# Performance work log

Hardware: AMD Instinct MI355X
Metric: run time of the kernel (lower is better)

## Reference

```python
import jax, jax.numpy as jnp
import numpy as np

# Poincare ball hyperbolic multi-head attention (hypll-style HMultiheadAttention)
C = 1.0          # ball curvature
SQRT_C = 1.0
EPS = 1e-7
B, S, E, H = 4, 1024, 512, 8
HD = E // H      # head_dim = 64


def _project_to_ball(u, scale=0.5):
    n = jnp.linalg.norm(u, axis=-1, keepdims=True)
    return u * (scale / (1.0 + n))  # guarantees ||x|| < scale < 1/sqrt(C)


def h_linear(x, z, r):
    """Poincare fully-connected layer (Shimizu et al. HNN++), as in hypll HLinear.
    x: [..., n] points in the ball, z: [n, m] weight directions, r: [m] bias."""
    x2 = jnp.sum(x * x, -1, keepdims=True)
    lam = 2.0 / jnp.maximum(1.0 - C * x2, EPS)          # conformal factor lambda_x
    zn = jnp.maximum(jnp.linalg.norm(z, axis=0), EPS)    # [m]
    xz = x @ z                                           # [..., m]
    two_cr = 2.0 * SQRT_C * r
    v = (2.0 * zn / SQRT_C) * jnp.arcsinh(
        SQRT_C * lam * xz / zn * jnp.cosh(two_cr) - (lam - 1.0) * jnp.sinh(two_cr)
    )
    v2 = jnp.sum(v * v, -1, keepdims=True)
    return v / (1.0 + jnp.sqrt(1.0 + C * v2))            # map back into the ball


def _split_heads(x):
    b, s, e = x.shape
    return x.reshape(b, s, H, HD).transpose(0, 2, 1, 3)  # [B,H,S,hd]; matches split(dim=-1)


def _h_attention(q, k, v):
    # similarity = -poincare_dist(q, k), pairwise via the arccosh closed form
    # (avoids materializing a [B,H,Sq,Sk,hd] mobius_add tensor)
    q2 = jnp.sum(q * q, -1)[..., :, None]                # [B,H,Sq,1]
    k2 = jnp.sum(k * k, -1)[..., None, :]                # [B,H,1,Sk]
    qk = jnp.einsum('bhqd,bhkd->bhqk', q, k)
    diff2 = jnp.maximum(q2 + k2 - 2.0 * qk, 0.0)
    denom = jnp.maximum((1.0 - C * q2) * (1.0 - C * k2), EPS)
    arg = 1.0 + 2.0 * C * diff2 / denom
    dist = jnp.arccosh(jnp.maximum(arg, 1.0 + EPS)) / SQRT_C
    w = jax.nn.softmax(-dist, axis=-1)                   # attention_activation
    # attention_midpoint: weighted Mobius gyromidpoint then half scalar-mul
    v2 = jnp.sum(v * v, -1)                              # [B,H,Sk]
    lam = 2.0 / jnp.maximum(1.0 - C * v2, EPS)
    num = jnp.einsum('bhqk,bhkd->bhqd', w * lam[..., None, :], v)
    den = jnp.einsum('bhqk,bhk->bhq', w, lam - 1.0)[..., None]
    m_bar = num / jnp.where(jnp.abs(den) < EPS, EPS, den)
    mn = jnp.maximum(jnp.linalg.norm(m_bar, axis=-1, keepdims=True), EPS)
    t = jnp.minimum(SQRT_C * mn, 1.0 - 1e-6)
    return jnp.tanh(0.5 * jnp.arctanh(t)) * m_bar / (SQRT_C * mn)  # (1/2) mobius-scalar-mul


def setup_inputs() -> dict:
    key = jax.random.key(0)
    ks = jax.random.split(key, 9)
    query = _project_to_ball(jax.random.normal(ks[0], (B, S, E), jnp.float32))
    key_t = _project_to_ball(jax.random.normal(ks[1], (B, S, E), jnp.float32))
    value = _project_to_ball(jax.random.normal(ks[2], (B, S, E), jnp.float32))
    scale = E ** -0.5
    zq = jax.random.normal(ks[3], (E, E), jnp.float32) * scale
    zk = jax.random.normal(ks[4], (E, E), jnp.float32) * scale
    zv = jax.random.normal(ks[5], (E, E), jnp.float32) * scale
    rq = jax.random.normal(ks[6], (E,), jnp.float32) * 0.01
    rk = jax.random.normal(ks[7], (E,), jnp.float32) * 0.01
    rv = jax.random.normal(ks[8], (E,), jnp.float32) * 0.01
    return {"query": query, "key": key_t, "value": value,
            "zq": zq, "rq": rq, "zk": zk, "rk": rk, "zv": zv, "rv": rv}


def reference(query, key, value, zq, rq, zk, rk, zv, rv):
    pq = h_linear(query, zq, rq)
    pk = h_linear(key, zk, rk)
    pv = h_linear(value, zv, rv)
    q, k, v = _split_heads(pq), _split_heads(pk), _split_heads(pv)
    out = _h_attention(q, k, v)                          # [B,H,S,hd]
    return out.transpose(0, 2, 1, 3).reshape(B, S, E)    # manifold.cat over heads
```

## Files before the change

kernel.cpp:

```cpp
#include <hip/hip_runtime.h>
#include <hip/hip_bf16.h>
#include <math.h>

#define EPSf 1e-7f
typedef unsigned short u16;
typedef __attribute__((ext_vector_type(8))) short bf16x8;
typedef __attribute__((ext_vector_type(4))) float f32x4;

__device__ __forceinline__ float bf2f(u16 u) {
  union { unsigned int i; float f; } x; x.i = ((unsigned int)u) << 16; return x.f;
}
__device__ __forceinline__ u16 f2bf(float f) {
  union { float f; unsigned int i; } x; x.f = f;
  unsigned int r = x.i + 0x7fffu + ((x.i >> 16) & 1u);
  return (u16)(r >> 16);
}
__device__ __forceinline__ void gll16(const void* g, void* l) {
  __builtin_amdgcn_global_load_lds((__attribute__((address_space(1))) void*)(g),
                                   (__attribute__((address_space(3))) void*)(l),
                                   16, 0, 0);
}

__global__ __launch_bounds__(256) void prep(
    const float* __restrict__ xq, const float* __restrict__ xk, const float* __restrict__ xv,
    const float* __restrict__ zq, const float* __restrict__ zk, const float* __restrict__ zv,
    u16* __restrict__ Xh, u16* __restrict__ Xl,
    float* __restrict__ Xn, float* __restrict__ Vn,
    u16* __restrict__ ZhT, u16* __restrict__ ZlT, float* __restrict__ Zn) {
  __shared__ float tile[64][68];
  const int t = threadIdx.x;
  if (blockIdx.x < 6144) {
    const int gr = blockIdx.x * 2 + (t >> 7);
    const int mat = gr >> 12, row = gr & 4095;
    const float* X = (mat == 0) ? xq : (mat == 1) ? xk : xv;
    const int f4 = t & 127;
    float4 x = ((const float4*)(X + (size_t)row * 512))[f4];
    u16 h0 = f2bf(x.x), h1 = f2bf(x.y), h2 = f2bf(x.z), h3 = f2bf(x.w);
    u16 l0 = f2bf(x.x - bf2f(h0)), l1 = f2bf(x.y - bf2f(h1));
    u16 l2 = f2bf(x.z - bf2f(h2)), l3 = f2bf(x.w - bf2f(h3));
    ((ushort4*)(Xh + (size_t)gr * 512))[f4] = make_ushort4(h0, h1, h2, h3);
    ((ushort4*)(Xl + (size_t)gr * 512))[f4] = make_ushort4(l0, l1, l2, l3);
    float a = fmaf(x.x, x.x, fmaf(x.y, x.y, fmaf(x.z, x.z, x.w * x.w)));
    a += __shfl_xor(a, 1);  a += __shfl_xor(a, 2);  a += __shfl_xor(a, 4);
    a += __shfl_xor(a, 8);  a += __shfl_xor(a, 16); a += __shfl_xor(a, 32);
    if ((t & 63) == 0) tile[0][t >> 6] = a;
    __syncthreads();
    if (t == 0)   { Xn[gr] = tile[0][0] + tile[0][1]; Vn[gr] = 0.f; }
    if (t == 128) { Xn[gr] = tile[0][2] + tile[0][3]; Vn[gr] = 0.f; }
  } else {
    const int idx = blockIdx.x - 6144;
    const int mat = idx >> 6;
    const int cg = (idx >> 3) & 7, kt = idx & 7;
    const int c0 = cg * 64;
    const float* Z = (mat == 0) ? zq : (mat == 1) ? zk : zv;
    {
      int kl = t >> 2;
      const float* src = Z + (size_t)(kt * 64 + kl) * 512 + c0 + (t & 3) * 16;
      #pragma unroll
      for (int j = 0; j < 4; ++j) {
        float4 v = *(const float4*)(src + 4 * j);
        *(float4*)&tile[kl][(t & 3) * 16 + 4 * j] = v;
      }
    }
    __syncthreads();
    const int cl = t >> 2, kg4 = t & 3;
    const size_t zo = (size_t)mat * 512 * 512;
    float csum = 0.f;
    #pragma unroll
    for (int jj = 0; jj < 4; ++jj) {
      u16 hb[4], lb[4];
      #pragma unroll
      for (int qq = 0; qq < 4; ++qq) {
        float zval = tile[kg4 * 16 + jj * 4 + qq][cl];
        csum = fmaf(zval, zval, csum);
        u16 hh = f2bf(zval);
        hb[qq] = hh;
        lb[qq] = f2bf(zval - bf2f(hh));
      }
      size_t o = zo + (size_t)(c0 + cl) * 512 + kt * 64 + kg4 * 16 + jj * 4;
      *(ushort4*)(ZhT + o) = make_ushort4(hb[0], hb[1], hb[2], hb[3]);
      *(ushort4*)(ZlT + o) = make_ushort4(lb[0], lb[1], lb[2], lb[3]);
    }
    csum += __shfl_xor(csum, 1);
    csum += __shfl_xor(csum, 2);
    if (kg4 == 0) atomicAdd(&Zn[mat * 512 + c0 + cl], csum);
  }
}

__global__ __launch_bounds__(256) void proj_gemm(
    const u16* __restrict__ Xh, const u16* __restrict__ Xl,
    const u16* __restrict__ ZhT, const u16* __restrict__ ZlT,
    const float* __restrict__ Xn, const float* __restrict__ Zn,
    const float* __restrict__ rq, const float* __restrict__ rk, const float* __restrict__ rv,
    float* __restrict__ Vtmp, float* __restrict__ Vn) {
  const int m0 = blockIdx.x * 64;
  const int n0 = blockIdx.y * 128;
  const int mat = blockIdx.z;
  const size_t xoff = (size_t)mat * 4096 * 512;
  const size_t zoff = (size_t)mat * 512 * 512;
  const int t = threadIdx.x, wv = t >> 6, lane = t & 63;
  const int l15 = lane & 15, quad = lane >> 4;
  const int wm = wv >> 1, wn = wv & 1;

  __shared__ __align__(16) u16 SM[12288];
  __shared__ float lams[64], lam1s[64], wmxs[128], wmys[128], wmzs[128];

  if (t < 64) {
    float x2 = Xn[mat * 4096 + m0 + t];
    float lam = 2.f / fmaxf(1.f - x2, EPSf);
    lams[t] = lam; lam1s[t] = lam - 1.f;
  }
  if (t < 128) {
    float zn = fmaxf(sqrtf(Zn[mat * 512 + n0 + t]), EPSf);
    const float* R = (mat == 0) ? rq : (mat == 1) ? rk : rv;
    float tr = 2.f * R[n0 + t];
    float e = expf(tr), ei = 1.f / e;
    wmxs[t] = 0.5f * (e + ei) / zn;
    wmys[t] = 0.5f * (e - ei);
    wmzs[t] = 2.f * zn;
  }

  f32x4 acc[2][4];
  #pragma unroll
  for (int i = 0; i < 2; ++i)
    #pragma unroll
    for (int j = 0; j < 4; ++j) acc[i][j] = (f32x4){0.f, 0.f, 0.f, 0.f};

  const u16* gs[6];
  u16* ld[6];
  #pragma unroll
  for (int ci = 0; ci < 6; ++ci) {
    int c = wv + 4 * ci;
    const u16* arr; int row0, lo;
    if (c < 4)       { arr = Xh + xoff;  row0 = m0 + 16 * c;        lo = c * 512; }
    else if (c < 8)  { arr = Xl + xoff;  row0 = m0 + 16 * (c - 4);  lo = 2048 + (c - 4) * 512; }
    else if (c < 16) { arr = ZhT + zoff; row0 = n0 + 16 * (c - 8);  lo = 4096 + (c - 8) * 512; }
    else             { arr = ZlT + zoff; row0 = n0 + 16 * (c - 16); lo = 8192 + (c - 16) * 512; }
    gs[ci] = arr + (size_t)(row0 + (lane >> 2)) * 512 + (lane & 3) * 8;
    ld[ci] = SM + lo;
  }

  for (int k0 = 0; k0 < 512; k0 += 32) {
    __syncthreads();
    #pragma unroll
    for (int ci = 0; ci < 6; ++ci) gll16(gs[ci] + k0, ld[ci]);
    __syncthreads();
    bf16x8 ah[2], al[2], bh_[4], bl_[4];
    #pragma unroll
    for (int i = 0; i < 2; ++i) {
      int ra = wm * 32 + i * 16 + l15;
      ah[i] = *(const bf16x8*)&SM[ra * 32 + quad * 8];
      al[i] = *(const bf16x8*)&SM[2048 + ra * 32 + quad * 8];
    }
    #pragma unroll
    for (int j = 0; j < 4; ++j) {
      int rb = wn * 64 + j * 16 + l15;
      bh_[j] = *(const bf16x8*)&SM[4096 + rb * 32 + quad * 8];
      bl_[j] = *(const bf16x8*)&SM[8192 + rb * 32 + quad * 8];
    }
    #pragma unroll
    for (int i = 0; i < 2; ++i)
      #pragma unroll
      for (int j = 0; j < 4; ++j) {
        acc[i][j] = __builtin_amdgcn_mfma_f32_16x16x32_bf16(ah[i], bh_[j], acc[i][j], 0, 0, 0);
        acc[i][j] = __builtin_amdgcn_mfma_f32_16x16x32_bf16(ah[i], bl_[j], acc[i][j], 0, 0, 0);
        acc[i][j] = __builtin_amdgcn_mfma_f32_16x16x32_bf16(al[i], bh_[j], acc[i][j], 0, 0, 0);
      }
  }

  #pragma unroll
  for (int i = 0; i < 2; ++i) {
    float rsum[4] = {0.f, 0.f, 0.f, 0.f};
    #pragma unroll
    for (int j = 0; j < 4; ++j) {
      int nl = wn * 64 + j * 16 + l15;
      float wx = wmxs[nl], wy = wmys[nl], wz = wmzs[nl];
      #pragma unroll
      for (int r = 0; r < 4; ++r) {
        int ml = wm * 32 + i * 16 + quad * 4 + r;
        float tt = lams[ml] * acc[i][j][r] * wx - lam1s[ml] * wy;
        float v = wz * logf(tt + sqrtf(fmaf(tt, tt, 1.f)));
        Vtmp[xoff + (size_t)(m0 + ml) * 512 + (n0 + nl)] = v;
        rsum[r] = fmaf(v, v, rsum[r]);
      }
    }
    #pragma unroll
    for (int r = 0; r < 4; ++r) {
      rsum[r] += __shfl_xor(rsum[r], 1);
      rsum[r] += __shfl_xor(rsum[r], 2);
      rsum[r] += __shfl_xor(rsum[r], 4);
      rsum[r] += __shfl_xor(rsum[r], 8);
    }
    if (l15 == 0) {
      #pragma unroll
      for (int r = 0; r < 4; ++r)
        atomicAdd(&Vn[mat * 4096 + m0 + wm * 32 + i * 16 + quad * 4 + r], rsum[r]);
    }
  }
}

__global__ __launch_bounds__(256) void pack(
    const float* __restrict__ Vtmp, const float* __restrict__ Vn,
    u16* __restrict__ Qh, u16* __restrict__ Kh, u16* __restrict__ VTb,
    float* __restrict__ q2a, float* __restrict__ aqa, float4* __restrict__ ksc) {
  __shared__ u16 tile[64][72];
  __shared__ float lams[64];
  const int t = threadIdx.x;
  if (blockIdx.x < 256) {
    const int mat = blockIdx.x >> 7;
    const int rb = blockIdx.x & 127;
    const int r = t >> 3, h = t & 7;
    const int row = rb * 32 + r;
    const size_t gr = (size_t)mat * 4096 + row;
    const float sc = 1.f / (1.f + sqrtf(1.f + Vn[gr]));
    const float* src = Vtmp + gr * 512 + h * 64;
    const int b = row >> 10, s = row & 1023;
    u16* dst = (mat ? Kh : Qh) + ((size_t)(b * 8 + h) * 1024 + s) * 64;
    float nrm = 0.f;
    #pragma unroll
    for (int j = 0; j < 16; ++j) {
      float4 x = *(const float4*)(src + 4 * j);
      u16 u0 = f2bf(x.x * sc), u1 = f2bf(x.y * sc), u2 = f2bf(x.z * sc), u3 = f2bf(x.w * sc);
      *(ushort4*)(dst + 4 * j) = make_ushort4(u0, u1, u2, u3);
      float f0 = bf2f(u0), f1 = bf2f(u1), f2 = bf2f(u2), f3 = bf2f(u3);
      nrm += f0 * f0 + f1 * f1 + f2 * f2 + f3 * f3;
    }
    const size_t so = (size_t)(b * 8 + h) * 1024 + s;
    if (mat == 0) { q2a[so] = nrm; aqa[so] = 1.f / fmaxf(1.f - nrm, EPSf); }
    else {
      float2 kk = make_float2(nrm, 2.f / fmaxf(1.f - nrm, EPSf));
      *(float2*)&ksc[so] = kk;
    }
  } else {
    const int idx = blockIdx.x - 256;
    const int bh = idx >> 4, st = idx & 15;
    const int b = bh >> 3, h = bh & 7;
    {
      const int s = t >> 2, dg = t & 3;
      const size_t gr = (size_t)2 * 4096 + b * 1024 + st * 64 + s;
      const float sc = 1.f / (1.f + sqrtf(1.f + Vn[gr]));
      const float* src = Vtmp + gr * 512 + h * 64 + dg * 16;
      float nrm = 0.f;
      #pragma unroll
      for (int j = 0; j < 4; ++j) {
        float4 x = *(const float4*)(src + 4 * j);
        u16 u0 = f2bf(x.x * sc), u1 = f2bf(x.y * sc), u2 = f2bf(x.z * sc), u3 = f2bf(x.w * sc);
        *(ushort4*)&tile[s][dg * 16 + 4 * j] = make_ushort4(u0, u1, u2, u3);
        float f0 = bf2f(u0), f1 = bf2f(u1), f2 = bf2f(u2), f3 = bf2f(u3);
        nrm += f0 * f0 + f1 * f1 + f2 * f2 + f3 * f3;
      }
      nrm += __shfl_xor(nrm, 1);
      nrm += __shfl_xor(nrm, 2);
      if (dg == 0) {
        float lam = 2.f / fmaxf(1.f - nrm, EPSf);
        lams[s] = lam;
        ((float*)&ksc[(size_t)bh * 1024 + st * 64 + s])[3] = lam - 1.f;
      }
    }
    __syncthreads();
    const int d = t >> 2, sg = t & 3;
    u16 ob[16];
    #pragma unroll
    for (int j = 0; j < 16; ++j) {
      int ss = sg * 16 + j;
      ob[j] = f2bf(bf2f(tile[ss][d]) * lams[ss]);
    }
    u16* dst = VTb + ((size_t)bh * 64 + d) * 1024 + st * 64 + sg * 16;
    #pragma unroll
    for (int j = 0; j < 4; ++j)
      *(ushort4*)(dst + 4 * j) = make_ushort4(ob[4 * j], ob[4 * j + 1], ob[4 * j + 2], ob[4 * j + 3]);
  }
}

__global__ __launch_bounds__(256, 3) void attn(
    const u16* __restrict__ Qh, const u16* __restrict__ Kh, const u16* __restrict__ VTb,
    const float* __restrict__ q2a, const float* __restrict__ aqa,
    const float4* __restrict__ ksc, float* __restrict__ out) {
  const int bh = blockIdx.x;
  const int b = bh >> 3, h = bh & 7;
  const int q0 = blockIdx.y * 32;
  const int t = threadIdx.x, wv = t >> 6, lane = t & 63;
  const int l15 = lane & 15, quad = lane >> 4;
  const int kq = wv;

  __shared__ __align__(16) u16 Ws[4][32 * 72];
  __shared__ float k2s[4][64], cks[4][64], l1s[4][64];
  __shared__ __align__(16) float nums[2][32][68];
  __shared__ float dens[2][32];

  const size_t qkoff = (size_t)bh * 65536;

  bf16x8 qf[2][2];
  float q2r[2], aqr[2];
  #pragma unroll
  for (int qs = 0; qs < 2; ++qs) {
    int qrow = q0 + qs * 16 + l15;
    const u16* qp = Qh + qkoff + (size_t)qrow * 64 + quad * 8;
    qf[qs][0] = *(const bf16x8*)qp;
    qf[qs][1] = *(const bf16x8*)(qp + 32);
    q2r[qs] = q2a[bh * 1024 + qrow];
    aqr[qs] = aqa[bh * 1024 + qrow];
  }

  f32x4 num[2][4];
  #pragma unroll
  for (int qs = 0; qs < 2; ++qs)
    #pragma unroll
    for (int tm = 0; tm < 4; ++tm) num[qs][tm] = (f32x4){0.f, 0.f, 0.f, 0.f};
  float denp[2] = {0.f, 0.f};

  #pragma unroll 1
  for (int i = 0; i < 4; ++i) {
    const int ktc = kq + 4 * i;
    float4 scur = ksc[bh * 1024 + ktc * 64 + lane];
    bf16x8 kcur[8];
    #pragma unroll
    for (int tn = 0; tn < 4; ++tn)
      #pragma unroll
      for (int ks = 0; ks < 2; ++ks)
        kcur[tn * 2 + ks] = *(const bf16x8*)(Kh + qkoff +
            (size_t)(ktc * 64 + tn * 16 + l15) * 64 + ks * 32 + quad * 8);
    k2s[wv][lane] = scur.x;
    cks[wv][lane] = scur.y;
    l1s[wv][lane] = scur.w;

    #pragma unroll
    for (int tn = 0; tn < 4; ++tn) {
      const float4 k2v = *(const float4*)&k2s[wv][tn * 16 + quad * 4];
      const float4 ckv = *(const float4*)&cks[wv][tn * 16 + quad * 4];
      const float4 l1v = *(const float4*)&l1s[wv][tn * 16 + quad * 4];
      #pragma unroll
      for (int qs = 0; qs < 2; ++qs) {
        f32x4 s = (f32x4){0.f, 0.f, 0.f, 0.f};
        s = __builtin_amdgcn_mfma_f32_16x16x32_bf16(kcur[tn * 2 + 0], qf[qs][0], s, 0, 0, 0);
        s = __builtin_amdgcn_mfma_f32_16x16x32_bf16(kcur[tn * 2 + 1], qf[qs][1], s, 0, 0, 0);
        unsigned up[2];
        #pragma unroll
        for (int pr = 0; pr < 2; ++pr) {
          float w2[2];
          #pragma unroll
          for (int e = 0; e < 2; ++e) {
            const int r = pr * 2 + e;
            float d2 = fmaxf(fmaf(-2.f, s[r], q2r[qs] + ((const float*)&k2v)[r]), 0.f);
            float u = fmaxf(d2 * ((const float*)&ckv)[r] * aqr[qs], EPSf);
            w2[e] = (1.f + u) - sqrtf(fmaf(u, u, u + u));
          }
          union { __hip_bfloat162 h2; unsigned u; } cv;
          cv.h2 = __float22bfloat162_rn(make_float2(w2[0], w2[1]));
          up[pr] = cv.u;
          float wlo = __uint_as_float(cv.u << 16);
          float whi = __uint_as_float(cv.u & 0xffff0000u);
          denp[qs] = fmaf(wlo, ((const float*)&l1v)[pr * 2 + 0], denp[qs]);
          denp[qs] = fmaf(whi, ((const float*)&l1v)[pr * 2 + 1], denp[qs]);
        }
        *(uint2*)&Ws[wv][(qs * 16 + l15) * 72 + tn * 16 + quad * 4] = make_uint2(up[0], up[1]);
      }
    }
    #pragma unroll
    for (int ks = 0; ks < 2; ++ks) {
      bf16x8 vfk[4];
      #pragma unroll
      for (int tm = 0; tm < 4; ++tm)
        vfk[tm] = *(const bf16x8*)(VTb + qkoff +
            (size_t)(tm * 16 + l15) * 1024 + ktc * 64 + ks * 32 + quad * 8);
      #pragma unroll
      for (int qs = 0; qs < 2; ++qs) {
        const bf16x8 wf = *(const bf16x8*)&Ws[wv][(qs * 16 + l15) * 72 + ks * 32 + quad * 8];
        #pragma unroll
        for (int tm = 0; tm < 4; ++tm)
          num[qs][tm] = __builtin_amdgcn_mfma_f32_16x16x32_bf16(
              vfk[tm], wf, num[qs][tm], 0, 0, 0);
      }
    }
  }

  #pragma unroll
  for (int qs = 0; qs < 2; ++qs) {
    denp[qs] += __shfl_xor(denp[qs], 16);
    denp[qs] += __shfl_xor(denp[qs], 32);
  }

  if (wv & 1) {
    const int buf = wv >> 1;
    #pragma unroll
    for (int qs = 0; qs < 2; ++qs) {
      #pragma unroll
      for (int tm = 0; tm < 4; ++tm)
        *(float4*)&nums[buf][qs * 16 + l15][tm * 16 + quad * 4] =
            make_float4(num[qs][tm][0], num[qs][tm][1], num[qs][tm][2], num[qs][tm][3]);
      if (quad == 0) dens[buf][qs * 16 + l15] = denp[qs];
    }
  }
  __syncthreads();
  if (!(wv & 1)) {
    const int buf = wv >> 1;
    #pragma unroll
    for (int qs = 0; qs < 2; ++qs) {
      #pragma unroll
      for (int tm = 0; tm < 4; ++tm) {
        float4 o = *(const float4*)&nums[buf][qs * 16 + l15][tm * 16 + quad * 4];
        num[qs][tm][0] += o.x; num[qs][tm][1] += o.y;
        num[qs][tm][2] += o.z; num[qs][tm][3] += o.w;
      }
      denp[qs] += dens[buf][qs * 16 + l15];
    }
  }
  if (wv == 2) {
    #pragma unroll
    for (int qs = 0; qs < 2; ++qs) {
      #pragma unroll
      for (int tm = 0; tm < 4; ++tm)
        *(float4*)&nums[1][qs * 16 + l15][tm * 16 + quad * 4] =
            make_float4(num[qs][tm][0], num[qs][tm][1], num[qs][tm][2], num[qs][tm][3]);
      if (quad == 0) dens[1][qs * 16 + l15] = denp[qs];
    }
  }
  __syncthreads();
  if (wv == 0) {
    #pragma unroll
    for (int qs = 0; qs < 2; ++qs) {
      #pragma unroll
      for (int tm = 0; tm < 4; ++tm) {
        float4 o = *(const float4*)&nums[1][qs * 16 + l15][tm * 16 + quad * 4];
        num[qs][tm][0] += o.x; num[qs][tm][1] += o.y;
        num[qs][tm][2] += o.z; num[qs][tm][3] += o.w;
      }
      float den = denp[qs] + dens[1][qs * 16 + l15];
      den = (fabsf(den) < EPSf) ? EPSf : den;
      float inv = 1.f / den;
      float mv[4][4];
      float p = 0.f;
      #pragma unroll
      for (int tm = 0; tm < 4; ++tm) {
        mv[tm][0] = num[qs][tm][0] * inv;
        mv[tm][1] = num[qs][tm][1] * inv;
        mv[tm][2] = num[qs][tm][2] * inv;
        mv[tm][3] = num[qs][tm][3] * inv;
        p = fmaf(mv[tm][0], mv[tm][0], p); p = fmaf(mv[tm][1], mv[tm][1], p);
        p = fmaf(mv[tm][2], mv[tm][2], p); p = fmaf(mv[tm][3], mv[tm][3], p);
      }
      p += __shfl_xor(p, 16);
      p += __shfl_xor(p, 32);
      float mn = sqrtf(p);
      float mnc = fmaxf(mn, EPSf);
      float tt2 = fminf(mnc, 1.f - 1e-6f);
      float scale = tt2 / ((1.f + sqrtf(fmaxf(1.f - tt2 * tt2, 0.f))) * mnc);
      const size_t qg = (size_t)b * 1024 + q0 + qs * 16 + l15;
      #pragma unroll
      for (int tm = 0; tm < 4; ++tm) {
        float4 o = make_float4(mv[tm][0] * scale, mv[tm][1] * scale,
                               mv[tm][2] * scale, mv[tm][3] * scale);
        *(float4*)(out + qg * 512 + h * 64 + tm * 16 + quad * 4) = o;
      }
    }
  }
}

extern "C" void kernel_launch(void* const* d_in, const int* in_sizes, int n_in,
                              void* d_out, int out_size, void* d_ws, size_t ws_size,
                              hipStream_t stream) {
  (void)in_sizes; (void)n_in; (void)out_size; (void)ws_size;
  const float* q  = (const float*)d_in[0];
  const float* k  = (const float*)d_in[1];
  const float* v  = (const float*)d_in[2];
  const float* zq = (const float*)d_in[3];
  const float* rq = (const float*)d_in[4];
  const float* zk = (const float*)d_in[5];
  const float* rk = (const float*)d_in[6];
  const float* zv = (const float*)d_in[7];
  const float* rv = (const float*)d_in[8];

  unsigned char* ws = (unsigned char*)d_ws;
  u16*   Xh   = (u16*)(ws + 0);
  u16*   Xl   = (u16*)(ws + 12582912);
  u16*   ZhT  = (u16*)(ws + 25165824);
  u16*   ZlT  = (u16*)(ws + 26738688);
  float* Vtmp = (float*)(ws + 28311552);
  float* Xn   = (float*)(ws + 53477376);
  float* Vn   = (float*)(ws + 53526528);
  float* Zn   = (float*)(ws + 53575680);
  u16*   Qh   = (u16*)(ws + 0);
  u16*   Kh   = (u16*)(ws + 4194304);
  u16*   VTb  = (u16*)(ws + 8388608);
  float* q2a  = (float*)(ws + 12582912);
  float* aqa  = (float*)(ws + 12713984);
  float4* ksc = (float4*)(ws + 12845056);

  hipMemsetAsync(Zn, 0, 6144, stream);
  prep<<<6336, 256, 0, stream>>>(q, k, v, zq, zk, zv, Xh, Xl, Xn, Vn, ZhT, ZlT, Zn);
  proj_gemm<<<dim3(64, 4, 3), 256, 0, stream>>>(Xh, Xl, ZhT, ZlT, Xn, Zn, rq, rk, rv, Vtmp, Vn);
  pack<<<768, 256, 0, stream>>>(Vtmp, Vn, Qh, Kh, VTb, q2a, aqa, ksc);
  attn<<<dim3(32, 32), 256, 0, stream>>>(Qh, Kh, VTb, q2a, aqa, ksc, (float*)d_out);
}
```

Baseline: 177.1 us.

## Prefetch next K tile in attention loop and coalesce Q/K pack writes

The attention loop now loads the next K tile fragments and key scalars into registers before computing on the current tile, so global loads overlap the MFMA work. The Q/K branch of the pack kernel is remapped so eight adjacent threads each handle eight elements of one row and write 16-byte packed stores. The row norm is then reduced with shuffles instead of one thread walking the whole 64-wide head row. The prefetch doubles K register usage, which may lower occupancy, and the last iteration issues a redundant reload.

```diff
diff --git a/kernel.cpp b/kernel.cpp
--- a/kernel.cpp
+++ b/kernel.cpp
@@ -208,28 +208,40 @@
   const int t = threadIdx.x;
   if (blockIdx.x < 256) {
     const int mat = blockIdx.x >> 7;
-    const int rb = blockIdx.x & 127;
-    const int r = t >> 3, h = t & 7;
-    const int row = rb * 32 + r;
-    const size_t gr = (size_t)mat * 4096 + row;
-    const float sc = 1.f / (1.f + sqrtf(1.f + Vn[gr]));
-    const float* src = Vtmp + gr * 512 + h * 64;
-    const int b = row >> 10, s = row & 1023;
-    u16* dst = (mat ? Kh : Qh) + ((size_t)(b * 8 + h) * 1024 + s) * 64;
-    float nrm = 0.f;
-    #pragma unroll
-    for (int j = 0; j < 16; ++j) {
-      float4 x = *(const float4*)(src + 4 * j);
-      u16 u0 = f2bf(x.x * sc), u1 = f2bf(x.y * sc), u2 = f2bf(x.z * sc), u3 = f2bf(x.w * sc);
-      *(ushort4*)(dst + 4 * j) = make_ushort4(u0, u1, u2, u3);
+    const int b   = (blockIdx.x >> 5) & 3;
+    const int h   = (blockIdx.x >> 2) & 7;
+    const int sq  = blockIdx.x & 3;
+    const int s8 = t >> 3, d8 = t & 7;
+    u16* outbase = (mat ? Kh : Qh) + (size_t)(b * 8 + h) * 65536;
+    #pragma unroll
+    for (int p = 0; p < 8; ++p) {
+      const int s = sq * 256 + p * 32 + s8;
+      const size_t gr = (size_t)mat * 4096 + b * 1024 + s;
+      const float sc = 1.f / (1.f + sqrtf(1.f + Vn[gr]));
+      const float* src = Vtmp + gr * 512 + h * 64 + d8 * 8;
+      float4 xa = *(const float4*)src;
+      float4 xb = *(const float4*)(src + 4);
+      u16 u0 = f2bf(xa.x * sc), u1 = f2bf(xa.y * sc), u2 = f2bf(xa.z * sc), u3 = f2bf(xa.w * sc);
+      u16 u4 = f2bf(xb.x * sc), u5 = f2bf(xb.y * sc), u6 = f2bf(xb.z * sc), u7 = f2bf(xb.w * sc);
+      uint4 pkd;
+      pkd.x = (unsigned)u0 | ((unsigned)u1 << 16);
+      pkd.y = (unsigned)u2 | ((unsigned)u3 << 16);
+      pkd.z = (unsigned)u4 | ((unsigned)u5 << 16);
+      pkd.w = (unsigned)u6 | ((unsigned)u7 << 16);
+      *(uint4*)(outbase + (size_t)s * 64 + d8 * 8) = pkd;
       float f0 = bf2f(u0), f1 = bf2f(u1), f2 = bf2f(u2), f3 = bf2f(u3);
-      nrm += f0 * f0 + f1 * f1 + f2 * f2 + f3 * f3;
-    }
-    const size_t so = (size_t)(b * 8 + h) * 1024 + s;
-    if (mat == 0) { q2a[so] = nrm; aqa[so] = 1.f / fmaxf(1.f - nrm, EPSf); }
-    else {
-      float2 kk = make_float2(nrm, 2.f / fmaxf(1.f - nrm, EPSf));
-      *(float2*)&ksc[so] = kk;
+      float f4 = bf2f(u4), f5 = bf2f(u5), f6 = bf2f(u6), f7 = bf2f(u7);
+      float nrm = f0*f0 + f1*f1 + f2*f2 + f3*f3 + f4*f4 + f5*f5 + f6*f6 + f7*f7;
+      nrm += __shfl_xor(nrm, 1);
+      nrm += __shfl_xor(nrm, 2);
+      nrm += __shfl_xor(nrm, 4);
+      if (d8 == 0) {
+        const size_t so = (size_t)(b * 8 + h) * 1024 + s;
+        if (mat == 0) { q2a[so] = nrm; aqa[so] = 1.f / fmaxf(1.f - nrm, EPSf); }
+        else {
+          *(float2*)&ksc[so] = make_float2(nrm, 2.f / fmaxf(1.f - nrm, EPSf));
+        }
+      }
     }
   } else {
     const int idx = blockIdx.x - 256;
@@ -309,17 +321,27 @@
     for (int tm = 0; tm < 4; ++tm) num[qs][tm] = (f32x4){0.f, 0.f, 0.f, 0.f};
   float denp[2] = {0.f, 0.f};
 
+  bf16x8 kcur[8];
+  #pragma unroll
+  for (int tn = 0; tn < 4; ++tn)
+    #pragma unroll
+    for (int ks = 0; ks < 2; ++ks)
+      kcur[tn * 2 + ks] = *(const bf16x8*)(Kh + qkoff +
+          (size_t)(kq * 64 + tn * 16 + l15) * 64 + ks * 32 + quad * 8);
+  float4 scur = ksc[bh * 1024 + kq * 64 + lane];
+
   #pragma unroll 1
   for (int i = 0; i < 4; ++i) {
     const int ktc = kq + 4 * i;
-    float4 scur = ksc[bh * 1024 + ktc * 64 + lane];
-    bf16x8 kcur[8];
+    const int kti = (i < 3) ? ktc + 4 : ktc;
+    bf16x8 knxt[8];
     #pragma unroll
     for (int tn = 0; tn < 4; ++tn)
       #pragma unroll
       for (int ks = 0; ks < 2; ++ks)
-        kcur[tn * 2 + ks] = *(const bf16x8*)(Kh + qkoff +
-            (size_t)(ktc * 64 + tn * 16 + l15) * 64 + ks * 32 + quad * 8);
+        knxt[tn * 2 + ks] = *(const bf16x8*)(Kh + qkoff +
+            (size_t)(kti * 64 + tn * 16 + l15) * 64 + ks * 32 + quad * 8);
+    float4 snxt = ksc[bh * 1024 + kti * 64 + lane];
     k2s[wv][lane] = scur.x;
     cks[wv][lane] = scur.y;
     l1s[wv][lane] = scur.w;
@@ -372,6 +394,9 @@
               vfk[tm], wf, num[qs][tm], 0, 0, 0);
       }
     }
+    #pragma unroll
+    for (int j = 0; j < 8; ++j) kcur[j] = knxt[j];
+    scur = snxt;
   }
 
   #pragma unroll
```

Result: faster. 172.9 us (-2.4%).
